# Optimization experiments

Hardware: AMD Instinct MI355X
Metric: run time of the kernel (lower is better)

## Reference

```python
import jax, jax.numpy as jnp
import numpy as np

NEG_SLOPE = 0.2
BN_EPS = 1e-5


def gat_conv(x, W_src, W_dst, att_src, att_dst, bias, src, dst, num_nodes):
    # PyG GATConv, heads=1, concat=True, self-loops already included in (src,dst)
    h_src = x @ W_src                      # [N, H]
    h_dst = x @ W_dst                      # [N, H]
    a_src = h_src @ att_src                # [N]
    a_dst = h_dst @ att_dst                # [N]
    e = jax.nn.leaky_relu(a_src[src] + a_dst[dst], NEG_SLOPE)   # [E]
    # segment softmax over incoming edges of each dst node
    m = jax.ops.segment_max(e, dst, num_segments=num_nodes)     # [N]
    p = jnp.exp(e - m[dst])
    denom = jax.ops.segment_sum(p, dst, num_segments=num_nodes) # [N]
    alpha = p / denom[dst]                                      # [E]
    msgs = alpha[:, None] * h_src[src]                           # [E, H]
    out = jax.ops.segment_sum(msgs, dst, num_segments=num_nodes)
    return out + bias


def setup_inputs() -> dict:
    key = jax.random.key(0)
    ks = jax.random.split(key, 20)
    N, D_IN, H1, H2, FC, C = 100000, 256, 128, 128, 64, 40
    E = 1600000
    inp = {}
    inp['x'] = jax.random.normal(ks[0], (N, D_IN), dtype=jnp.float32)
    inp['edge_index'] = jax.random.randint(ks[1], (2, E), 0, N, dtype=jnp.int64)
    s = 1.0 / np.sqrt(D_IN)
    inp['W1_src'] = jax.random.uniform(ks[2], (D_IN, H1), jnp.float32, -s, s)
    inp['W1_dst'] = jax.random.uniform(ks[3], (D_IN, H1), jnp.float32, -s, s)
    inp['att1_src'] = jax.random.normal(ks[4], (H1,), jnp.float32) * 0.1
    inp['att1_dst'] = jax.random.normal(ks[5], (H1,), jnp.float32) * 0.1
    inp['b1'] = jnp.zeros((H1,), jnp.float32)
    s = 1.0 / np.sqrt(H1)
    inp['W2_src'] = jax.random.uniform(ks[6], (H1, H2), jnp.float32, -s, s)
    inp['W2_dst'] = jax.random.uniform(ks[7], (H1, H2), jnp.float32, -s, s)
    inp['att2_src'] = jax.random.normal(ks[8], (H2,), jnp.float32) * 0.1
    inp['att2_dst'] = jax.random.normal(ks[9], (H2,), jnp.float32) * 0.1
    inp['b2'] = jnp.zeros((H2,), jnp.float32)
    s = 1.0 / np.sqrt(H2)
    inp['fc1_w'] = jax.random.uniform(ks[10], (H2, FC), jnp.float32, -s, s)
    inp['fc1_b'] = jax.random.uniform(ks[11], (FC,), jnp.float32, -s, s)
    inp['gamma'] = jnp.ones((FC,), jnp.float32)
    inp['beta'] = jnp.zeros((FC,), jnp.float32)
    s = 1.0 / np.sqrt(FC)
    inp['fc2_w'] = jax.random.uniform(ks[12], (FC, C), jnp.float32, -s, s)
    inp['fc2_b'] = jax.random.uniform(ks[13], (C,), jnp.float32, -s, s)
    return inp


def reference(x, edge_index, W1_src, W1_dst, att1_src, att1_dst, b1,
              W2_src, W2_dst, att2_src, att2_dst, b2,
              fc1_w, fc1_b, gamma, beta, fc2_w, fc2_b):
    N = x.shape[0]
    loops = jnp.arange(N, dtype=edge_index.dtype)
    src = jnp.concatenate([edge_index[0], loops])
    dst = jnp.concatenate([edge_index[1], loops])
    h = jax.nn.relu(gat_conv(x, W1_src, W1_dst, att1_src, att1_dst, b1, src, dst, N))
    h = jax.nn.relu(gat_conv(h, W2_src, W2_dst, att2_src, att2_dst, b2, src, dst, N))
    h = h @ fc1_w + fc1_b                   # [N, 64]
    mu = jnp.mean(h, axis=0)
    var = jnp.var(h, axis=0)
    h = (h - mu) * jax.lax.rsqrt(var + BN_EPS) * gamma + beta
    h = jax.nn.relu(h)
    h = h @ fc2_w + fc2_b                   # [N, C]
    return jax.nn.log_softmax(h, axis=-1)
```

## Files before the change

### kernel.cpp

```cpp
#include <hip/hip_runtime.h>
#include <cstddef>

#define LSLOPE 0.2f
#define BN_EPS 1e-5f

__device__ __forceinline__ float lrelu(float x) { return x > 0.f ? x : LSLOPE * x; }

using half4 = __attribute__((ext_vector_type(4))) _Float16;
using half8 = __attribute__((ext_vector_type(8))) _Float16;
using f32x4 = __attribute__((ext_vector_type(4))) float;

struct h2 { _Float16 h, l; };
__device__ __forceinline__ h2 split2h(float x) {
  h2 r;
  r.h = (_Float16)x;
  r.l = (_Float16)(x - (float)r.h);
  return r;
}

__device__ __forceinline__ unsigned short f2bf(float x) {
  unsigned u = __float_as_uint(x);
  unsigned r = (u + 0x7fffu + ((u >> 16) & 1u)) >> 16;
  return (unsigned short)r;
}
__device__ __forceinline__ float bflo(unsigned int u) { return __uint_as_float(u << 16); }
__device__ __forceinline__ float bfhi(unsigned int u) { return __uint_as_float(u & 0xffff0000u); }

__global__ void bfrag_k(const float* __restrict__ B, _Float16* __restrict__ bh,
                        _Float16* __restrict__ bl, int K, int M) {
  int t = blockIdx.x * 256 + threadIdx.x;
  int KB = K >> 5;
  int total = (M >> 4) * KB * 64;
  if (t >= total) return;
  int lane = t & 63;
  int ckb  = t >> 6;
  int c  = ckb / KB, kb = ckb % KB;
  int mr = lane & 15, quad = lane >> 4;
  int col = c * 16 + mr;
  size_t obase = (size_t)t * 8;
#pragma unroll
  for (int j = 0; j < 8; ++j) {
    int k = kb * 32 + quad * 8 + j;
    h2 s = split2h(B[(size_t)k * M + col]);
    bh[obase + j] = s.h;
    bl[obase + j] = s.l;
  }
}

template<int MCOLS>
__global__ __launch_bounds__(256) void gemm3h_k(const float* __restrict__ A,
                                                const _Float16* __restrict__ Bh,
                                                const _Float16* __restrict__ Bl,
                                                float* __restrict__ Cf,
                                                unsigned short* __restrict__ Cbf,
                                                const float* __restrict__ attv,
                                                float* __restrict__ asrc,
                                                int N, int K,
                                                const float* __restrict__ bias) {
  constexpr int CT = MCOLS / 16;
  __shared__ __align__(16) _Float16 sAh[128 * 32];
  __shared__ __align__(16) _Float16 sAl[128 * 32];
  const int tid  = threadIdx.x;
  const int row0 = blockIdx.x * 128;
  const int wv   = tid >> 6;
  const int lane = tid & 63;
  const int quad = lane >> 4;
  const int mr   = lane & 15;
  const int KB   = K >> 5;

  f32x4 acc[2][CT];
#pragma unroll
  for (int r = 0; r < 2; ++r)
#pragma unroll
    for (int c = 0; c < CT; ++c) acc[r][c] = (f32x4){0.f, 0.f, 0.f, 0.f};

  for (int kb = 0; kb < KB; ++kb) {
    const int kk = kb << 5;
#pragma unroll
    for (int cc = 0; cc < 4; ++cc) {
      int s = tid + cc * 256;
      int r = s >> 3, kc = (s & 7) << 2;
      float4 v = make_float4(0.f, 0.f, 0.f, 0.f);
      int gr = row0 + r;
      if (gr < N) v = *(const float4*)&A[(size_t)gr * K + kk + kc];
      h2 s0 = split2h(v.x);
      h2 s1 = split2h(v.y);
      h2 s2 = split2h(v.z);
      h2 s3 = split2h(v.w);
      half4 h4, l4;
      h4[0] = s0.h; h4[1] = s1.h; h4[2] = s2.h; h4[3] = s3.h;
      l4[0] = s0.l; l4[1] = s1.l; l4[2] = s2.l; l4[3] = s3.l;
      int off = r * 32 + ((kc + r * 8) & 31);
      *(half4*)&sAh[off] = h4;
      *(half4*)&sAl[off] = l4;
    }
    __syncthreads();

    half8 ah[2], al[2];
#pragma unroll
    for (int r = 0; r < 2; ++r) {
      int row = wv * 32 + r * 16 + mr;
      int off = row * 32 + ((quad + row) & 3) * 8;
      ah[r] = *(const half8*)&sAh[off];
      al[r] = *(const half8*)&sAl[off];
    }
    const _Float16* bb_h = Bh + ((size_t)kb * 64 + lane) * 8;
    const _Float16* bb_l = Bl + ((size_t)kb * 64 + lane) * 8;
    const size_t cstride = (size_t)KB * 512;
#pragma unroll
    for (int c0 = 0; c0 < CT; c0 += 4) {
      half8 bh4[4], bl4[4];
#pragma unroll
      for (int c = 0; c < 4; ++c) {
        size_t o = (size_t)(c0 + c) * cstride;
        bh4[c] = *(const half8*)&bb_h[o];
        bl4[c] = *(const half8*)&bb_l[o];
      }
#pragma unroll
      for (int r = 0; r < 2; ++r)
#pragma unroll
        for (int c = 0; c < 4; ++c) {
          f32x4 a = acc[r][c0 + c];
          a = __builtin_amdgcn_mfma_f32_16x16x32_f16(al[r], bh4[c], a, 0, 0, 0);
          a = __builtin_amdgcn_mfma_f32_16x16x32_f16(ah[r], bl4[c], a, 0, 0, 0);
          a = __builtin_amdgcn_mfma_f32_16x16x32_f16(ah[r], bh4[c], a, 0, 0, 0);
          acc[r][c0 + c] = a;
        }
    }
    __syncthreads();
  }

  float pa[2][4];
#pragma unroll
  for (int r = 0; r < 2; ++r)
#pragma unroll
    for (int q = 0; q < 4; ++q) pa[r][q] = 0.f;

#pragma unroll
  for (int r = 0; r < 2; ++r)
#pragma unroll
    for (int c = 0; c < CT; ++c) {
      float av = attv ? attv[c * 16 + mr] : 0.f;
#pragma unroll
      for (int q = 0; q < 4; ++q) {
        int grow = row0 + wv * 32 + r * 16 + quad * 4 + q;
        float val = acc[r][c][q];
        if (bias) val += bias[c * 16 + mr];
        if (grow < N) {
          int gcol = c * 16 + mr;
          if (Cf)  Cf[(size_t)grow * MCOLS + gcol] = val;
          if (Cbf) Cbf[(size_t)grow * 128 + gcol] = f2bf(val);
        }
        if (attv) pa[r][q] = fmaf(val, av, pa[r][q]);
      }
    }
  if (attv) {
#pragma unroll
    for (int r = 0; r < 2; ++r)
#pragma unroll
      for (int q = 0; q < 4; ++q) {
        float p2 = pa[r][q];
        p2 += __shfl_xor(p2, 1, 64);
        p2 += __shfl_xor(p2, 2, 64);
        p2 += __shfl_xor(p2, 4, 64);
        p2 += __shfl_xor(p2, 8, 64);
        int grow = row0 + wv * 32 + r * 16 + quad * 4 + q;
        if (mr == 0 && grow < N) asrc[grow] = p2;
      }
  }
}

__global__ __launch_bounds__(256) void matvec_k(const float* __restrict__ A, const float* __restrict__ v,
                                                float* __restrict__ out, int R, int K) {
  int w = (blockIdx.x * blockDim.x + threadIdx.x) >> 6;
  int lane = threadIdx.x & 63;
  if (w >= R) return;
  const float* row = A + (size_t)w * K;
  float s = 0.f;
  for (int k = lane; k < K; k += 64) s = fmaf(row[k], v[k], s);
#pragma unroll
  for (int off = 32; off; off >>= 1) s += __shfl_xor(s, off, 64);
  if (lane == 0) out[w] = s;
}

__global__ void deg_count_k(const int* __restrict__ edst, int E, int N, int* __restrict__ deg) {
  int i = blockIdx.x * 256 + threadIdx.x;
  if (i >= E + N) return;
  int d = (i < E) ? edst[i] : (i - E);
  atomicAdd(&deg[d], 1);
}

__global__ __launch_bounds__(1024) void scan1_k(const int* __restrict__ deg, int n,
                                                int* __restrict__ ex, int* __restrict__ bsum) {
  __shared__ int sm[1024];
  int t = threadIdx.x;
  int idx = blockIdx.x * 1024 + t;
  int v = (idx < n) ? deg[idx] : 0;
  sm[t] = v;
  __syncthreads();
  for (int off = 1; off < 1024; off <<= 1) {
    int tv = (t >= off) ? sm[t - off] : 0;
    __syncthreads();
    sm[t] += tv;
    __syncthreads();
  }
  if (idx < n) ex[idx] = sm[t] - v;
  if (t == 1023) bsum[blockIdx.x] = sm[t];
}

__global__ void scan2_k(int* __restrict__ bsum, int nb) {
  if (threadIdx.x == 0 && blockIdx.x == 0) {
    int run = 0;
    for (int b = 0; b < nb; ++b) { int x = bsum[b]; bsum[b] = run; run += x; }
  }
}

__global__ void scan3_k(int* __restrict__ ex, const int* __restrict__ bsum, int n, int total,
                        int* __restrict__ cursor) {
  int idx = blockIdx.x * 256 + threadIdx.x;
  if (idx < n) {
    int v = ex[idx] + bsum[idx >> 10];
    ex[idx] = v;
    cursor[idx] = v;
  }
  if (idx == 0) ex[n] = total;
}

__global__ void scatter_range_k(const int* __restrict__ esrc, const int* __restrict__ edst,
                                int E, int N, int d0, int d1,
                                int* __restrict__ cursor, int* __restrict__ csr_src) {
  int i = blockIdx.x * 256 + threadIdx.x;
  if (i >= E + N) return;
  int d = (i < E) ? edst[i] : (i - E);
  if (d < d0 || d >= d1) return;
  int s = (i < E) ? esrc[i] : d;
  int pos = atomicAdd(&cursor[d], 1);
  csr_src[pos] = s;
}

__global__ __launch_bounds__(256) void gat_agg_k(const unsigned short* __restrict__ hbf,
                                                 const float* __restrict__ a_src,
                                                 const float* __restrict__ a_dst, const int* __restrict__ rowstart,
                                                 const int* __restrict__ csr_src, const float* __restrict__ bias,
                                                 float* __restrict__ outp, int N) {
  int w = (blockIdx.x * blockDim.x + threadIdx.x) >> 6;
  int lane = threadIdx.x & 63;
  if (w >= N) return;
  int s0 = rowstart[w];
  int s1 = rowstart[w + 1];
  int deg = s1 - s0;
  float ad = a_dst[w];

  int sA = 0;
  float eA = -3.0e38f;
  if (lane < deg) {
    sA = csr_src[s0 + lane];
    eA = lrelu(a_src[sA] + ad);
  }
  float m = eA;
  for (int j = s0 + 64 + lane; j < s1; j += 64) {
    int s = csr_src[j];
    m = fmaxf(m, lrelu(a_src[s] + ad));
  }
#pragma unroll
  for (int off = 32; off; off >>= 1) m = fmaxf(m, __shfl_xor(m, off, 64));

  float preg = (lane < deg) ? __expf(eA - m) : 0.f;
  float den = preg;
  for (int j = s0 + 64 + lane; j < s1; j += 64) {
    int s = csr_src[j];
    den += __expf(lrelu(a_src[s] + ad) - m);
  }
#pragma unroll
  for (int off = 32; off; off >>= 1) den += __shfl_xor(den, off, 64);
  float inv = 1.f / den;

  const int q  = lane >> 4;
  const int sl = lane & 15;
  const uint4* hrow4 = (const uint4*)hbf;
  float acc[8];
#pragma unroll
  for (int i = 0; i < 8; ++i) acc[i] = 0.f;

  int lim  = deg < 64 ? deg : 64;
  int lim4 = (lim + 3) & ~3;
  for (int jj = 0; jj < lim4; jj += 4) {
    int e = jj + q;
    int s = __shfl(sA, e, 64);
    float wgt = __shfl(preg, e, 64) * inv;
    uint4 u = hrow4[(size_t)s * 16 + sl];
    acc[0] = fmaf(wgt, bflo(u.x), acc[0]);
    acc[1] = fmaf(wgt, bfhi(u.x), acc[1]);
    acc[2] = fmaf(wgt, bflo(u.y), acc[2]);
    acc[3] = fmaf(wgt, bfhi(u.y), acc[3]);
    acc[4] = fmaf(wgt, bflo(u.z), acc[4]);
    acc[5] = fmaf(wgt, bfhi(u.z), acc[5]);
    acc[6] = fmaf(wgt, bflo(u.w), acc[6]);
    acc[7] = fmaf(wgt, bfhi(u.w), acc[7]);
  }
  for (int j = s0 + 64 + q; j < s1; j += 4) {
    int s = csr_src[j];
    float wgt = __expf(lrelu(a_src[s] + ad) - m) * inv;
    uint4 u = hrow4[(size_t)s * 16 + sl];
    acc[0] = fmaf(wgt, bflo(u.x), acc[0]);
    acc[1] = fmaf(wgt, bfhi(u.x), acc[1]);
    acc[2] = fmaf(wgt, bflo(u.y), acc[2]);
    acc[3] = fmaf(wgt, bfhi(u.y), acc[3]);
    acc[4] = fmaf(wgt, bflo(u.z), acc[4]);
    acc[5] = fmaf(wgt, bfhi(u.z), acc[5]);
    acc[6] = fmaf(wgt, bflo(u.w), acc[6]);
    acc[7] = fmaf(wgt, bfhi(u.w), acc[7]);
  }
#pragma unroll
  for (int i = 0; i < 8; ++i) {
    acc[i] += __shfl_xor(acc[i], 16, 64);
    acc[i] += __shfl_xor(acc[i], 32, 64);
  }
  if (q == 0) {
    float4 b0 = *(const float4*)&bias[8 * sl];
    float4 b1 = *(const float4*)&bias[8 * sl + 4];
    float4 o0, o1;
    o0.x = fmaxf(acc[0] + b0.x, 0.f);
    o0.y = fmaxf(acc[1] + b0.y, 0.f);
    o0.z = fmaxf(acc[2] + b0.z, 0.f);
    o0.w = fmaxf(acc[3] + b0.w, 0.f);
    o1.x = fmaxf(acc[4] + b1.x, 0.f);
    o1.y = fmaxf(acc[5] + b1.y, 0.f);
    o1.z = fmaxf(acc[6] + b1.z, 0.f);
    o1.w = fmaxf(acc[7] + b1.w, 0.f);
    float* orow = outp + (size_t)w * 128 + 8 * sl;
    *(float4*)orow = o0;
    *(float4*)(orow + 4) = o1;
  }
}

__global__ __launch_bounds__(256) void bn_stats_k(const float* __restrict__ z, int N,
                                                  float* __restrict__ sums, float* __restrict__ sumsq) {
  __shared__ float ls[256], lq[256];
  int col = threadIdx.x & 63;
  int rg = threadIdx.x >> 6;
  float s = 0.f, q = 0.f;
  for (int r = blockIdx.x * 4 + rg; r < N; r += gridDim.x * 4) {
    float v = z[(size_t)r * 64 + col];
    s += v;
    q = fmaf(v, v, q);
  }
  ls[threadIdx.x] = s;
  lq[threadIdx.x] = q;
  __syncthreads();
  if (threadIdx.x < 64) {
    s = ls[col] + ls[col + 64] + ls[col + 128] + ls[col + 192];
    q = lq[col] + lq[col + 64] + lq[col + 128] + lq[col + 192];
    atomicAdd(&sums[col], s);
    atomicAdd(&sumsq[col], q);
  }
}

__global__ void bn_finalize_k(const float* __restrict__ sums, const float* __restrict__ sumsq,
                              const float* __restrict__ gamma, const float* __restrict__ beta,
                              int N, float* __restrict__ scale, float* __restrict__ shift) {
  int c = threadIdx.x;
  if (c >= 64) return;
  float mean = sums[c] / (float)N;
  float var = sumsq[c] / (float)N - mean * mean;
  float rs = rsqrtf(var + BN_EPS);
  float sc = gamma[c] * rs;
  scale[c] = sc;
  shift[c] = beta[c] - mean * sc;
}

__global__ __launch_bounds__(256) void fc2_lsm_k(const float* __restrict__ z, const float* __restrict__ scale,
                                                 const float* __restrict__ shift, const float* __restrict__ w,
                                                 const float* __restrict__ b, float* __restrict__ out, int N) {
  int n = blockIdx.x * 256 + threadIdx.x;
  if (n >= N) return;
  float o[40];
#pragma unroll
  for (int c = 0; c < 40; ++c) o[c] = b[c];
  const float* zr = z + (size_t)n * 64;
  for (int k = 0; k < 64; ++k) {
    float v = fmaxf(fmaf(zr[k], scale[k], shift[k]), 0.f);
#pragma unroll
    for (int c = 0; c < 40; ++c) o[c] = fmaf(v, w[k * 40 + c], o[c]);
  }
  float mx = o[0];
#pragma unroll
  for (int c = 1; c < 40; ++c) mx = fmaxf(mx, o[c]);
  float s = 0.f;
#pragma unroll
  for (int c = 0; c < 40; ++c) s += __expf(o[c] - mx);
  float ls = __logf(s);
  float* orow = out + (size_t)n * 40;
#pragma unroll
  for (int c = 0; c < 40; ++c) orow[c] = o[c] - mx - ls;
}

static inline char* al16(char* p) { return (char*)(((size_t)p + 15) & ~(size_t)15); }

extern "C" void kernel_launch(void* const* d_in, const int* in_sizes, int n_in,
                              void* d_out, int out_size, void* d_ws, size_t ws_size,
                              hipStream_t stream) {
  const float* x     = (const float*)d_in[0];
  const int*   eidx  = (const int*)d_in[1];
  const float* W1s   = (const float*)d_in[2];
  const float* W1d   = (const float*)d_in[3];
  const float* att1s = (const float*)d_in[4];
  const float* att1d = (const float*)d_in[5];
  const float* b1    = (const float*)d_in[6];
  const float* W2s   = (const float*)d_in[7];
  const float* W2d   = (const float*)d_in[8];
  const float* att2s = (const float*)d_in[9];
  const float* att2d = (const float*)d_in[10];
  const float* b2    = (const float*)d_in[11];
  const float* fc1w  = (const float*)d_in[12];
  const float* fc1b  = (const float*)d_in[13];
  const float* gamma = (const float*)d_in[14];
  const float* beta  = (const float*)d_in[15];
  const float* fc2w  = (const float*)d_in[16];
  const float* fc2b  = (const float*)d_in[17];
  float* out = (float*)d_out;

  const int N  = in_sizes[0] / 256;
  const int E  = in_sizes[1] / 2;
  const int ET = E + N;
  const int DIN = 256, H1 = 128;

  char* p = (char*)d_ws;
  float* hB = (float*)p;               p += (size_t)N * 128 * 4;
  float* hF = (float*)p;               p += (size_t)N * 64 * 4;
  unsigned short* bhA = (unsigned short*)p; p += (size_t)N * 128 * 2;
  int* deg      = (int*)p;     p += (size_t)N * 4;
  int* rowstart = (int*)p;     p += (size_t)(N + 1) * 4;
  int* cursor   = (int*)p;     p += (size_t)N * 4;
  int* csr_src  = (int*)p;     p += (size_t)ET * 4;
  float* a_src  = (float*)p;   p += (size_t)N * 4;
  float* a_dst  = (float*)p;   p += (size_t)N * 4;
  float* wvd1   = (float*)p;   p += 256 * 4;
  float* wvd2   = (float*)p;   p += 128 * 4;
  float* sums   = (float*)p;   p += 64 * 4;
  float* sumsq  = (float*)p;   p += 64 * 4;
  float* scale  = (float*)p;   p += 64 * 4;
  float* shift  = (float*)p;   p += 64 * 4;
  int* bsum     = (int*)p;     p += 256 * 4;
  p = al16(p);
  _Float16* B1h = (_Float16*)p; p += (size_t)256 * 128 * 2;
  _Float16* B1l = (_Float16*)p; p += (size_t)256 * 128 * 2;
  _Float16* B2h = (_Float16*)p; p += (size_t)128 * 128 * 2;
  _Float16* B2l = (_Float16*)p; p += (size_t)128 * 128 * 2;
  _Float16* Bfh = (_Float16*)p; p += (size_t)128 * 64 * 2;
  _Float16* Bfl = (_Float16*)p; p += (size_t)128 * 64 * 2;

  const int* esrc = eidx;
  const int* edst = eidx + E;

  hipMemsetAsync(deg, 0, (size_t)N * 4, stream);
  deg_count_k<<<(ET + 255) / 256, 256, 0, stream>>>(edst, E, N, deg);
  int nb = (N + 1023) / 1024;
  scan1_k<<<nb, 1024, 0, stream>>>(deg, N, rowstart, bsum);
  scan2_k<<<1, 64, 0, stream>>>(bsum, nb);
  scan3_k<<<(N + 255) / 256, 256, 0, stream>>>(rowstart, bsum, N, ET, cursor);
  {
    const int NR = 8;
    int step = (N + NR - 1) / NR;
    for (int r = 0; r < NR; ++r) {
      int d0 = r * step;
      int d1 = d0 + step < N ? d0 + step : N;
      scatter_range_k<<<(ET + 255) / 256, 256, 0, stream>>>(esrc, edst, E, N, d0, d1, cursor, csr_src);
    }
  }

  bfrag_k<<<16, 256, 0, stream>>>(W1s, B1h, B1l, 256, 128);
  bfrag_k<<<8, 256, 0, stream>>>(W2s, B2h, B2l, 128, 128);
  bfrag_k<<<4, 256, 0, stream>>>(fc1w, Bfh, Bfl, 128, 64);
  matvec_k<<<64, 256, 0, stream>>>(W1d, att1d, wvd1, 256, 128);
  matvec_k<<<32, 256, 0, stream>>>(W2d, att2d, wvd2, 128, 128);

  const int gemm_blocks = (N + 127) / 128;

  gemm3h_k<128><<<gemm_blocks, 256, 0, stream>>>(x, B1h, B1l, (float*)nullptr, bhA, att1s, a_src,
                                                 N, DIN, (const float*)nullptr);
  matvec_k<<<(N + 3) / 4, 256, 0, stream>>>(x, wvd1, a_dst, N, DIN);
  gat_agg_k<<<(N + 3) / 4, 256, 0, stream>>>(bhA, a_src, a_dst, rowstart, csr_src, b1, hB, N);

  gemm3h_k<128><<<gemm_blocks, 256, 0, stream>>>(hB, B2h, B2l, (float*)nullptr, bhA, att2s, a_src,
                                                 N, H1, (const float*)nullptr);
  matvec_k<<<(N + 3) / 4, 256, 0, stream>>>(hB, wvd2, a_dst, N, H1);
  gat_agg_k<<<(N + 3) / 4, 256, 0, stream>>>(bhA, a_src, a_dst, rowstart, csr_src, b2, hB, N);

  gemm3h_k<64><<<gemm_blocks, 256, 0, stream>>>(hB, Bfh, Bfl, hF, (unsigned short*)nullptr,
                                                (const float*)nullptr, (float*)nullptr, N, H1, fc1b);
  hipMemsetAsync(sums, 0, 128 * sizeof(float), stream);
  bn_stats_k<<<512, 256, 0, stream>>>(hF, N, sums, sumsq);
  bn_finalize_k<<<1, 64, 0, stream>>>(sums, sumsq, gamma, beta, N, scale, shift);
  fc2_lsm_k<<<(N + 255) / 256, 256, 0, stream>>>(hF, scale, shift, fc2w, fc2b, out, N);
}
```

Baseline: 764.3 us.

## Double-buffer GEMM A tiles, pre-split aggregation output, fuse layer-2 a_dst matvec

The first GEMM kernel now double-buffers its shared-memory A tiles, so the next tile's global loads are issued before the current tile's MFMAs. The GAT aggregation epilogue now writes its ReLU output directly as fp16 hi/lo halves. A new GEMM variant loads those halves without splitting them again. For layer 1, the aggregation also computes the layer-2 a_dst dot product, which removes a separate matvec pass over the hidden features. The cost is double the LDS per block, which may lower occupancy, plus extra epilogue work in the aggregation kernel.

```diff
diff --git a/kernel.cpp b/kernel.cpp
--- a/kernel.cpp
+++ b/kernel.cpp
@@ -58,8 +58,8 @@
                                                 int N, int K,
                                                 const float* __restrict__ bias) {
   constexpr int CT = MCOLS / 16;
-  __shared__ __align__(16) _Float16 sAh[128 * 32];
-  __shared__ __align__(16) _Float16 sAl[128 * 32];
+  __shared__ __align__(16) _Float16 sAh[2][128 * 32];
+  __shared__ __align__(16) _Float16 sAl[2][128 * 32];
   const int tid  = threadIdx.x;
   const int row0 = blockIdx.x * 128;
   const int wv   = tid >> 6;
@@ -68,41 +68,56 @@
   const int mr   = lane & 15;
   const int KB   = K >> 5;
 
+  int srow[4], skc[4], soff[4];
+  bool sok[4];
+#pragma unroll
+  for (int cc = 0; cc < 4; ++cc) {
+    int s = tid + cc * 256;
+    srow[cc] = s >> 3;
+    skc[cc]  = (s & 7) << 2;
+    soff[cc] = srow[cc] * 32 + ((skc[cc] + srow[cc] * 8) & 31);
+    sok[cc]  = (row0 + srow[cc]) < N;
+  }
+
   f32x4 acc[2][CT];
 #pragma unroll
   for (int r = 0; r < 2; ++r)
 #pragma unroll
     for (int c = 0; c < CT; ++c) acc[r][c] = (f32x4){0.f, 0.f, 0.f, 0.f};
 
+  float4 pf[4];
+#pragma unroll
+  for (int cc = 0; cc < 4; ++cc)
+    pf[cc] = sok[cc] ? *(const float4*)&A[(size_t)(row0 + srow[cc]) * K + skc[cc]]
+                     : make_float4(0.f, 0.f, 0.f, 0.f);
+#pragma unroll
+  for (int cc = 0; cc < 4; ++cc) {
+    h2 s0 = split2h(pf[cc].x), s1 = split2h(pf[cc].y), s2 = split2h(pf[cc].z), s3 = split2h(pf[cc].w);
+    half4 h4, l4;
+    h4[0] = s0.h; h4[1] = s1.h; h4[2] = s2.h; h4[3] = s3.h;
+    l4[0] = s0.l; l4[1] = s1.l; l4[2] = s2.l; l4[3] = s3.l;
+    *(half4*)&sAh[0][soff[cc]] = h4;
+    *(half4*)&sAl[0][soff[cc]] = l4;
+  }
+  __syncthreads();
+
   for (int kb = 0; kb < KB; ++kb) {
-    const int kk = kb << 5;
-#pragma unroll
-    for (int cc = 0; cc < 4; ++cc) {
-      int s = tid + cc * 256;
-      int r = s >> 3, kc = (s & 7) << 2;
-      float4 v = make_float4(0.f, 0.f, 0.f, 0.f);
-      int gr = row0 + r;
-      if (gr < N) v = *(const float4*)&A[(size_t)gr * K + kk + kc];
-      h2 s0 = split2h(v.x);
-      h2 s1 = split2h(v.y);
-      h2 s2 = split2h(v.z);
-      h2 s3 = split2h(v.w);
-      half4 h4, l4;
-      h4[0] = s0.h; h4[1] = s1.h; h4[2] = s2.h; h4[3] = s3.h;
-      l4[0] = s0.l; l4[1] = s1.l; l4[2] = s2.l; l4[3] = s3.l;
-      int off = r * 32 + ((kc + r * 8) & 31);
-      *(half4*)&sAh[off] = h4;
-      *(half4*)&sAl[off] = l4;
-    }
-    __syncthreads();
+    const int cur = kb & 1, nxt = cur ^ 1;
+    if (kb + 1 < KB) {
+      const int kk = (kb + 1) << 5;
+#pragma unroll
+      for (int cc = 0; cc < 4; ++cc)
+        pf[cc] = sok[cc] ? *(const float4*)&A[(size_t)(row0 + srow[cc]) * K + kk + skc[cc]]
+                         : make_float4(0.f, 0.f, 0.f, 0.f);
+    }
 
     half8 ah[2], al[2];
 #pragma unroll
     for (int r = 0; r < 2; ++r) {
       int row = wv * 32 + r * 16 + mr;
       int off = row * 32 + ((quad + row) & 3) * 8;
-      ah[r] = *(const half8*)&sAh[off];
-      al[r] = *(const half8*)&sAl[off];
+      ah[r] = *(const half8*)&sAh[cur][off];
+      al[r] = *(const half8*)&sAl[cur][off];
     }
     const _Float16* bb_h = Bh + ((size_t)kb * 64 + lane) * 8;
     const _Float16* bb_l = Bl + ((size_t)kb * 64 + lane) * 8;
@@ -126,6 +141,164 @@
           a = __builtin_amdgcn_mfma_f32_16x16x32_f16(ah[r], bh4[c], a, 0, 0, 0);
           acc[r][c0 + c] = a;
         }
+    }
+    if (kb + 1 < KB) {
+#pragma unroll
+      for (int cc = 0; cc < 4; ++cc) {
+        h2 s0 = split2h(pf[cc].x), s1 = split2h(pf[cc].y), s2 = split2h(pf[cc].z), s3 = split2h(pf[cc].w);
+        half4 h4, l4;
+        h4[0] = s0.h; h4[1] = s1.h; h4[2] = s2.h; h4[3] = s3.h;
+        l4[0] = s0.l; l4[1] = s1.l; l4[2] = s2.l; l4[3] = s3.l;
+        *(half4*)&sAh[nxt][soff[cc]] = h4;
+        *(half4*)&sAl[nxt][soff[cc]] = l4;
+      }
+    }
+    __syncthreads();
+  }
+
+  float pa[2][4];
+#pragma unroll
+  for (int r = 0; r < 2; ++r)
+#pragma unroll
+    for (int q = 0; q < 4; ++q) pa[r][q] = 0.f;
+
+#pragma unroll
+  for (int r = 0; r < 2; ++r)
+#pragma unroll
+    for (int c = 0; c < CT; ++c) {
+      float av = attv ? attv[c * 16 + mr] : 0.f;
+#pragma unroll
+      for (int q = 0; q < 4; ++q) {
+        int grow = row0 + wv * 32 + r * 16 + quad * 4 + q;
+        float val = acc[r][c][q];
+        if (bias) val += bias[c * 16 + mr];
+        if (grow < N) {
+          int gcol = c * 16 + mr;
+          if (Cf)  Cf[(size_t)grow * MCOLS + gcol] = val;
+          if (Cbf) Cbf[(size_t)grow * 128 + gcol] = f2bf(val);
+        }
+        if (attv) pa[r][q] = fmaf(val, av, pa[r][q]);
+      }
+    }
+  if (attv) {
+#pragma unroll
+    for (int r = 0; r < 2; ++r)
+#pragma unroll
+      for (int q = 0; q < 4; ++q) {
+        float p2 = pa[r][q];
+        p2 += __shfl_xor(p2, 1, 64);
+        p2 += __shfl_xor(p2, 2, 64);
+        p2 += __shfl_xor(p2, 4, 64);
+        p2 += __shfl_xor(p2, 8, 64);
+        int grow = row0 + wv * 32 + r * 16 + quad * 4 + q;
+        if (mr == 0 && grow < N) asrc[grow] = p2;
+      }
+  }
+}
+
+template<int MCOLS>
+__global__ __launch_bounds__(256) void gemm3p_k(const _Float16* __restrict__ Ah,
+                                                const _Float16* __restrict__ Al,
+                                                const _Float16* __restrict__ Bh,
+                                                const _Float16* __restrict__ Bl,
+                                                float* __restrict__ Cf,
+                                                unsigned short* __restrict__ Cbf,
+                                                const float* __restrict__ attv,
+                                                float* __restrict__ asrc,
+                                                int N, int K,
+                                                const float* __restrict__ bias) {
+  constexpr int CT = MCOLS / 16;
+  __shared__ __align__(16) _Float16 sAh[2][128 * 32];
+  __shared__ __align__(16) _Float16 sAl[2][128 * 32];
+  const int tid  = threadIdx.x;
+  const int row0 = blockIdx.x * 128;
+  const int wv   = tid >> 6;
+  const int lane = tid & 63;
+  const int quad = lane >> 4;
+  const int mr   = lane & 15;
+  const int KB   = K >> 5;
+
+  int srow[2], sk8[2], soff[2];
+  bool sok[2];
+#pragma unroll
+  for (int cc = 0; cc < 2; ++cc) {
+    int s = tid + cc * 256;
+    srow[cc] = s >> 2;
+    sk8[cc]  = (s & 3) << 3;
+    soff[cc] = srow[cc] * 32 + ((sk8[cc] + srow[cc] * 8) & 31);
+    sok[cc]  = (row0 + srow[cc]) < N;
+  }
+
+  f32x4 acc[2][CT];
+#pragma unroll
+  for (int r = 0; r < 2; ++r)
+#pragma unroll
+    for (int c = 0; c < CT; ++c) acc[r][c] = (f32x4){0.f, 0.f, 0.f, 0.f};
+
+  uint4 ph[2], pl[2];
+  const uint4 z4 = make_uint4(0u, 0u, 0u, 0u);
+#pragma unroll
+  for (int cc = 0; cc < 2; ++cc) {
+    size_t go = (size_t)(row0 + srow[cc]) * K + sk8[cc];
+    ph[cc] = sok[cc] ? *(const uint4*)&Ah[go] : z4;
+    pl[cc] = sok[cc] ? *(const uint4*)&Al[go] : z4;
+  }
+#pragma unroll
+  for (int cc = 0; cc < 2; ++cc) {
+    *(uint4*)&sAh[0][soff[cc]] = ph[cc];
+    *(uint4*)&sAl[0][soff[cc]] = pl[cc];
+  }
+  __syncthreads();
+
+  for (int kb = 0; kb < KB; ++kb) {
+    const int cur = kb & 1, nxt = cur ^ 1;
+    if (kb + 1 < KB) {
+      const int kk = (kb + 1) << 5;
+#pragma unroll
+      for (int cc = 0; cc < 2; ++cc) {
+        size_t go = (size_t)(row0 + srow[cc]) * K + kk + sk8[cc];
+        ph[cc] = sok[cc] ? *(const uint4*)&Ah[go] : z4;
+        pl[cc] = sok[cc] ? *(const uint4*)&Al[go] : z4;
+      }
+    }
+
+    half8 ah[2], al[2];
+#pragma unroll
+    for (int r = 0; r < 2; ++r) {
+      int row = wv * 32 + r * 16 + mr;
+      int off = row * 32 + ((quad + row) & 3) * 8;
+      ah[r] = *(const half8*)&sAh[cur][off];
+      al[r] = *(const half8*)&sAl[cur][off];
+    }
+    const _Float16* bb_h = Bh + ((size_t)kb * 64 + lane) * 8;
+    const _Float16* bb_l = Bl + ((size_t)kb * 64 + lane) * 8;
+    const size_t cstride = (size_t)KB * 512;
+#pragma unroll
+    for (int c0 = 0; c0 < CT; c0 += 4) {
+      half8 bh4[4], bl4[4];
+#pragma unroll
+      for (int c = 0; c < 4; ++c) {
+        size_t o = (size_t)(c0 + c) * cstride;
+        bh4[c] = *(const half8*)&bb_h[o];
+        bl4[c] = *(const half8*)&bb_l[o];
+      }
+#pragma unroll
+      for (int r = 0; r < 2; ++r)
+#pragma unroll
+        for (int c = 0; c < 4; ++c) {
+          f32x4 a = acc[r][c0 + c];
+          a = __builtin_amdgcn_mfma_f32_16x16x32_f16(al[r], bh4[c], a, 0, 0, 0);
+          a = __builtin_amdgcn_mfma_f32_16x16x32_f16(ah[r], bl4[c], a, 0, 0, 0);
+          a = __builtin_amdgcn_mfma_f32_16x16x32_f16(ah[r], bh4[c], a, 0, 0, 0);
+          acc[r][c0 + c] = a;
+        }
+    }
+    if (kb + 1 < KB) {
+#pragma unroll
+      for (int cc = 0; cc < 2; ++cc) {
+        *(uint4*)&sAh[nxt][soff[cc]] = ph[cc];
+        *(uint4*)&sAl[nxt][soff[cc]] = pl[cc];
+      }
     }
     __syncthreads();
   }
@@ -242,7 +415,9 @@
                                                  const float* __restrict__ a_src,
                                                  const float* __restrict__ a_dst, const int* __restrict__ rowstart,
                                                  const int* __restrict__ csr_src, const float* __restrict__ bias,
-                                                 float* __restrict__ outp, int N) {
+                                                 _Float16* __restrict__ oh, _Float16* __restrict__ ol,
+                                                 const float* __restrict__ wvd, float* __restrict__ ad_out,
+                                                 int N) {
   int w = (blockIdx.x * blockDim.x + threadIdx.x) >> 6;
   int lane = threadIdx.x & 63;
   if (w >= N) return;
@@ -319,18 +494,36 @@
   if (q == 0) {
     float4 b0 = *(const float4*)&bias[8 * sl];
     float4 b1 = *(const float4*)&bias[8 * sl + 4];
-    float4 o0, o1;
-    o0.x = fmaxf(acc[0] + b0.x, 0.f);
-    o0.y = fmaxf(acc[1] + b0.y, 0.f);
-    o0.z = fmaxf(acc[2] + b0.z, 0.f);
-    o0.w = fmaxf(acc[3] + b0.w, 0.f);
-    o1.x = fmaxf(acc[4] + b1.x, 0.f);
-    o1.y = fmaxf(acc[5] + b1.y, 0.f);
-    o1.z = fmaxf(acc[6] + b1.z, 0.f);
-    o1.w = fmaxf(acc[7] + b1.w, 0.f);
-    float* orow = outp + (size_t)w * 128 + 8 * sl;
-    *(float4*)orow = o0;
-    *(float4*)(orow + 4) = o1;
+    float v[8];
+    v[0] = fmaxf(acc[0] + b0.x, 0.f);
+    v[1] = fmaxf(acc[1] + b0.y, 0.f);
+    v[2] = fmaxf(acc[2] + b0.z, 0.f);
+    v[3] = fmaxf(acc[3] + b0.w, 0.f);
+    v[4] = fmaxf(acc[4] + b1.x, 0.f);
+    v[5] = fmaxf(acc[5] + b1.y, 0.f);
+    v[6] = fmaxf(acc[6] + b1.z, 0.f);
+    v[7] = fmaxf(acc[7] + b1.w, 0.f);
+    half8 vh, vl;
+#pragma unroll
+    for (int i = 0; i < 8; ++i) {
+      h2 s = split2h(v[i]);
+      vh[i] = s.h;
+      vl[i] = s.l;
+    }
+    size_t base = (size_t)w * 128 + 8 * sl;
+    *(half8*)&oh[base] = vh;
+    *(half8*)&ol[base] = vl;
+    if (wvd) {
+      float4 w0 = *(const float4*)&wvd[8 * sl];
+      float4 w1 = *(const float4*)&wvd[8 * sl + 4];
+      float dd = v[0] * w0.x + v[1] * w0.y + v[2] * w0.z + v[3] * w0.w
+               + v[4] * w1.x + v[5] * w1.y + v[6] * w1.z + v[7] * w1.w;
+      dd += __shfl_xor(dd, 1, 64);
+      dd += __shfl_xor(dd, 2, 64);
+      dd += __shfl_xor(dd, 4, 64);
+      dd += __shfl_xor(dd, 8, 64);
+      if (sl == 0) ad_out[w] = dd;
+    }
   }
 }
 
@@ -426,15 +619,17 @@
   const int DIN = 256, H1 = 128;
 
   char* p = (char*)d_ws;
-  float* hB = (float*)p;               p += (size_t)N * 128 * 4;
-  float* hF = (float*)p;               p += (size_t)N * 64 * 4;
   unsigned short* bhA = (unsigned short*)p; p += (size_t)N * 128 * 2;
+  _Float16* hAh = (_Float16*)p;  p += (size_t)N * 128 * 2;
+  _Float16* hAl = (_Float16*)p;  p += (size_t)N * 128 * 2;
+  float* hF = (float*)p;         p += (size_t)N * 64 * 4;
   int* deg      = (int*)p;     p += (size_t)N * 4;
   int* rowstart = (int*)p;     p += (size_t)(N + 1) * 4;
   int* cursor   = (int*)p;     p += (size_t)N * 4;
   int* csr_src  = (int*)p;     p += (size_t)ET * 4;
   float* a_src  = (float*)p;   p += (size_t)N * 4;
   float* a_dst  = (float*)p;   p += (size_t)N * 4;
+  float* a_dst2 = (float*)p;   p += (size_t)N * 4;
   float* wvd1   = (float*)p;   p += 256 * 4;
   float* wvd2   = (float*)p;   p += 128 * 4;
   float* sums   = (float*)p;   p += 64 * 4;
@@ -480,14 +675,15 @@
   gemm3h_k<128><<<gemm_blocks, 256, 0, stream>>>(x, B1h, B1l, (float*)nullptr, bhA, att1s, a_src,
                                                  N, DIN, (const float*)nullptr);
   matvec_k<<<(N + 3) / 4, 256, 0, stream>>>(x, wvd1, a_dst, N, DIN);
-  gat_agg_k<<<(N + 3) / 4, 256, 0, stream>>>(bhA, a_src, a_dst, rowstart, csr_src, b1, hB, N);
-
-  gemm3h_k<128><<<gemm_blocks, 256, 0, stream>>>(hB, B2h, B2l, (float*)nullptr, bhA, att2s, a_src,
+  gat_agg_k<<<(N + 3) / 4, 256, 0, stream>>>(bhA, a_src, a_dst, rowstart, csr_src, b1,
+                                             hAh, hAl, wvd2, a_dst2, N);
+
+  gemm3p_k<128><<<gemm_blocks, 256, 0, stream>>>(hAh, hAl, B2h, B2l, (float*)nullptr, bhA, att2s, a_src,
                                                  N, H1, (const float*)nullptr);
-  matvec_k<<<(N + 3) / 4, 256, 0, stream>>>(hB, wvd2, a_dst, N, H1);
-  gat_agg_k<<<(N + 3) / 4, 256, 0, stream>>>(bhA, a_src, a_dst, rowstart, csr_src, b2, hB, N);
-
-  gemm3h_k<64><<<gemm_blocks, 256, 0, stream>>>(hB, Bfh, Bfl, hF, (unsigned short*)nullptr,
+  gat_agg_k<<<(N + 3) / 4, 256, 0, stream>>>(bhA, a_src, a_dst2, rowstart, csr_src, b2,
+                                             hAh, hAl, (const float*)nullptr, (float*)nullptr, N);
+
+  gemm3p_k<64><<<gemm_blocks, 256, 0, stream>>>(hAh, hAl, Bfh, Bfl, hF, (unsigned short*)nullptr,
                                                 (const float*)nullptr, (float*)nullptr, N, H1, fc1b);
   hipMemsetAsync(sums, 0, 128 * sizeof(float), stream);
   bn_stats_k<<<512, 256, 0, stream>>>(hF, N, sums, sumsq);
```

After: 763.9 us. No clear change (-0.0%).
